# Performance work log

Measured on AMD Instinct MI355X. Metric: run time of the kernel, lower is better.

The kernel has to match this reference:

```python
import jax, jax.numpy as jnp
import numpy as np

K = 3          # kernel size
STRIDE = 1
PAD = 1
DIL = 1


def setup_inputs() -> dict:
    key = jax.random.key(0)
    k1, k2, k3 = jax.random.split(key, 3)
    N, Cin, H, W = 8, 128, 64, 64
    Cout = 128
    x = jax.random.normal(k1, (N, Cin, H, W), dtype=jnp.float32)
    # offset channels: 2 * deformable_groups * K*K = 18, interleaved (dy, dx) per tap
    offset = jax.random.normal(k2, (N, 2 * K * K, H, W), dtype=jnp.float32)
    weight = jax.random.normal(k3, (Cout, Cin, K, K), dtype=jnp.float32) / np.sqrt(Cin * K * K)
    return {"x": x, "offset": offset, "weight": weight}


def _deform_conv(x, offset, weight):
    N, Cin, H, W = x.shape
    Cout = weight.shape[0]
    KK = K * K
    Ho, Wo = offset.shape[2], offset.shape[3]

    off = offset.reshape(N, KK, 2, Ho, Wo)
    dy = off[:, :, 0]  # [N, KK, Ho, Wo]
    dx = off[:, :, 1]

    kh = jnp.repeat(jnp.arange(K), K).astype(x.dtype)   # [KK]
    kw = jnp.tile(jnp.arange(K), K).astype(x.dtype)     # [KK]
    base_i = (jnp.arange(Ho) * STRIDE - PAD).astype(x.dtype)  # [Ho]
    base_j = (jnp.arange(Wo) * STRIDE - PAD).astype(x.dtype)  # [Wo]

    # Sampling positions: [N, KK, Ho, Wo]
    py = base_i[None, None, :, None] + (kh * DIL)[None, :, None, None] + dy
    px = base_j[None, None, None, :] + (kw * DIL)[None, :, None, None] + dx

    y0 = jnp.floor(py)
    x0 = jnp.floor(px)
    wy1 = py - y0
    wx1 = px - x0
    wy0 = 1.0 - wy1
    wx0 = 1.0 - wx1
    y0i = y0.astype(jnp.int32)
    x0i = x0.astype(jnp.int32)
    y1i = y0i + 1
    x1i = x0i + 1

    x_flat = x.reshape(N, Cin, H * W)

    def gather(yi, xi):
        # zero-padding outside the image
        mask = ((yi >= 0) & (yi < H) & (xi >= 0) & (xi < W)).astype(x.dtype)
        idx = jnp.clip(yi, 0, H - 1) * W + jnp.clip(xi, 0, W - 1)  # [N,KK,Ho,Wo]
        v = jnp.take_along_axis(x_flat, idx.reshape(N, 1, -1), axis=2)  # [N,Cin,KK*Ho*Wo]
        v = v.reshape(N, Cin, KK, Ho, Wo)
        return v * mask[:, None]

    sampled = (gather(y0i, x0i) * (wy0 * wx0)[:, None]
               + gather(y0i, x1i) * (wy0 * wx1)[:, None]
               + gather(y1i, x0i) * (wy1 * wx0)[:, None]
               + gather(y1i, x1i) * (wy1 * wx1)[:, None])  # [N,Cin,KK,Ho,Wo]

    w = weight.reshape(Cout, Cin, KK)
    return jnp.einsum('nckij,ock->noij', sampled, w)


def reference(x, offset, weight):
    return _deform_conv(x, offset, weight)
```

## Files before the change

kernel.cpp:

```cpp
#include <hip/hip_runtime.h>


#define H  64
#define W  64
#define CIN 128
#define COUT 128
#define NB 8
#define KK 9

typedef short bf16x8 __attribute__((ext_vector_type(8)));
typedef float f32x4  __attribute__((ext_vector_type(4)));

__device__ __forceinline__ unsigned short f2bf(float f) {
    unsigned u = __builtin_bit_cast(unsigned, f);
    u += 0x7FFFu + ((u >> 16) & 1u);
    return (unsigned short)(u >> 16);
}
__device__ __forceinline__ float lo_f(unsigned u) { return __builtin_bit_cast(float, u << 16); }
__device__ __forceinline__ float hi_f(unsigned u) { return __builtin_bit_cast(float, u & 0xFFFF0000u); }

__global__ void prep_weight(const float* __restrict__ w, unsigned short* __restrict__ wt) {
    int idx = blockIdx.x * 256 + threadIdx.x;
    if (idx >= KK * COUT * CIN) return;
    int kk = idx / (COUT * CIN);
    int r  = idx - kk * (COUT * CIN);
    int co = r >> 7;
    int c  = r & 127;
    wt[idx] = f2bf(w[(co * CIN + c) * KK + kk]);
}

__global__ void prep_x(const float* __restrict__ x, unsigned short* __restrict__ xt) {
    __shared__ float tile[CIN][W + 1];
    int b = blockIdx.x;
    int n = b >> 6, y = b & 63;
    int t = threadIdx.x;
    int l = t & 63, g = t >> 6;
    const float* src = x + ((size_t)n * CIN * H + y) * W;
    #pragma unroll
    for (int i = 0; i < 32; ++i) {
        int c = g * 32 + i;
        tile[c][l] = src[(size_t)c * H * W + l];
    }
    __syncthreads();
    int xp = t >> 2;
    int cb = (t & 3) * 32;
    unsigned short* dst = xt + (((size_t)(n * H + y) * W + xp) * CIN + cb);
    unsigned rr[16];
    #pragma unroll
    for (int i = 0; i < 16; ++i) {
        float v0 = tile[cb + 2 * i][xp];
        float v1 = tile[cb + 2 * i + 1][xp];
        rr[i] = (unsigned)f2bf(v0) | ((unsigned)f2bf(v1) << 16);
    }
    #pragma unroll
    for (int i = 0; i < 4; ++i)
        ((uint4*)dst)[i] = make_uint4(rr[4*i], rr[4*i+1], rr[4*i+2], rr[4*i+3]);
}

__global__ __launch_bounds__(512, 4) void deform_main(
        const float* __restrict__ offs, const unsigned short* __restrict__ xt,
        const unsigned short* __restrict__ wt, float* __restrict__ out) {
    __shared__ __attribute__((aligned(16))) unsigned short samp[64][CIN + 8];
    __shared__ __attribute__((aligned(16))) unsigned short wts[COUT][CIN + 8];

    int b = blockIdx.x;
    int n = b >> 6, ho = b & 63;
    int t = threadIdx.x;
    int lane = t & 63, wv = t >> 6;
    int lm = lane & 15, lq = lane >> 4;
    int prow = ((wv >> 1) << 4) + lm;
    int cobase = (wv & 1) << 6;

    f32x4 acc[4] = {{0,0,0,0},{0,0,0,0},{0,0,0,0},{0,0,0,0}};

    int p  = t >> 3;
    int cb = (t & 7) << 4;
    const float* offbase = offs + (((size_t)n * 2 * KK) * H + ho) * W + p;

    for (int kk = 0; kk < KK; ++kk) {
        {
            int co = t >> 2;
            int ch = (t & 3) << 5;
            const uint4* src = (const uint4*)(wt + (((size_t)kk * COUT + co) << 7) + ch);
            uint4* dst = (uint4*)&wts[co][ch];
            #pragma unroll
            for (int i = 0; i < 4; ++i) dst[i] = src[i];
        }
        {
            float dy = offbase[(size_t)(2 * kk) * H * W];
            float dx = offbase[(size_t)(2 * kk + 1) * H * W];
            float py = (float)(ho - 1 + kk / 3) + dy;
            float px = (float)(p  - 1 + kk % 3) + dx;
            float y0f = floorf(py), x0f = floorf(px);
            float wy1 = py - y0f, wx1 = px - x0f;
            float wy0 = 1.f - wy1, wx0 = 1.f - wx1;
            int y0 = (int)y0f, x0 = (int)x0f;
            int y1 = y0 + 1, x1 = x0 + 1;
            bool vy0 = (unsigned)y0 < (unsigned)H, vy1 = (unsigned)y1 < (unsigned)H;
            bool vx0 = (unsigned)x0 < (unsigned)W, vx1 = (unsigned)x1 < (unsigned)W;
            float w00 = (vy0 && vx0) ? wy0 * wx0 : 0.f;
            float w01 = (vy0 && vx1) ? wy0 * wx1 : 0.f;
            float w10 = (vy1 && vx0) ? wy1 * wx0 : 0.f;
            float w11 = (vy1 && vx1) ? wy1 * wx1 : 0.f;
            int yc0 = min(max(y0, 0), H - 1), yc1 = min(max(y1, 0), H - 1);
            int xc0 = min(max(x0, 0), W - 1), xc1 = min(max(x1, 0), W - 1);
            const unsigned short* r0 = xt + (size_t)(n * H + yc0) * W * CIN + cb;
            const unsigned short* r1 = xt + (size_t)(n * H + yc1) * W * CIN + cb;
            const unsigned short* b00 = r0 + xc0 * CIN;
            const unsigned short* b01 = r0 + xc1 * CIN;
            const unsigned short* b10 = r1 + xc0 * CIN;
            const unsigned short* b11 = r1 + xc1 * CIN;
            #pragma unroll
            for (int j = 0; j < 2; ++j) {
                uint4 q00 = *(const uint4*)(b00 + 8 * j);
                uint4 q01 = *(const uint4*)(b01 + 8 * j);
                uint4 q10 = *(const uint4*)(b10 + 8 * j);
                uint4 q11 = *(const uint4*)(b11 + 8 * j);
                const unsigned* a0 = (const unsigned*)&q00;
                const unsigned* a1 = (const unsigned*)&q01;
                const unsigned* a2 = (const unsigned*)&q10;
                const unsigned* a3 = (const unsigned*)&q11;
                unsigned rr[4];
                #pragma unroll
                for (int i = 0; i < 4; ++i) {
                    float v0 = w00*lo_f(a0[i]) + w01*lo_f(a1[i]) + w10*lo_f(a2[i]) + w11*lo_f(a3[i]);
                    float v1 = w00*hi_f(a0[i]) + w01*hi_f(a1[i]) + w10*hi_f(a2[i]) + w11*hi_f(a3[i]);
                    rr[i] = (unsigned)f2bf(v0) | ((unsigned)f2bf(v1) << 16);
                }
                *(uint4*)&samp[p][cb + 8 * j] = make_uint4(rr[0], rr[1], rr[2], rr[3]);
            }
        }
        __syncthreads();
        #pragma unroll
        for (int ct = 0; ct < 4; ++ct) {
            bf16x8 a = *(const bf16x8*)&samp[prow][(ct << 5) + (lq << 3)];
            #pragma unroll
            for (int nt = 0; nt < 4; ++nt) {
                bf16x8 bf = *(const bf16x8*)&wts[cobase + (nt << 4) + lm][(ct << 5) + (lq << 3)];
                acc[nt] = __builtin_amdgcn_mfma_f32_16x16x32_bf16(a, bf, acc[nt], 0, 0, 0);
            }
        }
        __syncthreads();
    }
    int wo = ((wv >> 1) << 4) + (lq << 2);
    #pragma unroll
    for (int nt = 0; nt < 4; ++nt) {
        int co = cobase + (nt << 4) + lm;
        *(f32x4*)(out + (((size_t)(n * COUT + co) * H + ho) * W + wo)) = acc[nt];
    }
}

extern "C" void kernel_launch(void* const* d_in, const int* in_sizes, int n_in,
                              void* d_out, int out_size, void* d_ws, size_t ws_size,
                              hipStream_t stream) {
    const float* x      = (const float*)d_in[0];
    const float* offset = (const float*)d_in[1];
    const float* weight = (const float*)d_in[2];
    float* out = (float*)d_out;

    unsigned short* xt = (unsigned short*)d_ws;
    unsigned short* wt = (unsigned short*)((char*)d_ws + (size_t)NB*H*W*CIN*2);

    hipLaunchKernelGGL(prep_weight, dim3((KK*COUT*CIN + 255) / 256), dim3(256), 0, stream,
                       weight, wt);
    hipLaunchKernelGGL(prep_x, dim3(NB * H), dim3(256), 0, stream, x, xt);
    hipLaunchKernelGGL(deform_main, dim3(NB * H), dim3(512), 0, stream,
                       offset, xt, wt, out);
}
```

Baseline: 112.5 us.

## Pre-swizzle weights into MFMA fragment layout and double-buffer sampled tile

Weights are pre-packed into the per-lane MFMA B-fragment layout so the main kernel reads them directly from global/L2 instead of staging a weight tile in LDS each tap. The sampled-activation LDS buffer is double-buffered, which removes one barrier per tap, and the next tap's offsets are prefetched. Blocks are halved to 256 threads covering 32 output columns, which doubles the grid and cuts LDS use to raise occupancy. In exchange, each block re-reads the weights from cache, and the prep_x store pattern is changed.

```diff
diff --git a/kernel.cpp b/kernel.cpp
--- a/kernel.cpp
+++ b/kernel.cpp
@@ -19,14 +19,20 @@
 __device__ __forceinline__ float lo_f(unsigned u) { return __builtin_bit_cast(float, u << 16); }
 __device__ __forceinline__ float hi_f(unsigned u) { return __builtin_bit_cast(float, u & 0xFFFF0000u); }
 
-__global__ void prep_weight(const float* __restrict__ w, unsigned short* __restrict__ wt) {
-    int idx = blockIdx.x * 256 + threadIdx.x;
-    if (idx >= KK * COUT * CIN) return;
-    int kk = idx / (COUT * CIN);
-    int r  = idx - kk * (COUT * CIN);
-    int co = r >> 7;
-    int c  = r & 127;
-    wt[idx] = f2bf(w[(co * CIN + c) * KK + kk]);
+__global__ void prep_weight(const float* __restrict__ w, unsigned short* __restrict__ wtf) {
+    int id = blockIdx.x * 256 + threadIdx.x;
+    int lane = id & 63;
+    int ct = (id >> 6) & 3;
+    int nt = (id >> 8) & 7;
+    int kk = id >> 11;
+    if (kk >= KK) return;
+    int co = nt * 16 + (lane & 15);
+    int c0 = ct * 32 + (lane >> 4) * 8;
+    unsigned short v[8];
+    #pragma unroll
+    for (int j = 0; j < 8; ++j)
+        v[j] = f2bf(w[((size_t)co * CIN + c0 + j) * KK + kk]);
+    *(uint4*)(wtf + (size_t)id * 8) = *(const uint4*)v;
 }
 
 __global__ void prep_x(const float* __restrict__ x, unsigned short* __restrict__ xt) {
@@ -42,111 +48,111 @@
         tile[c][l] = src[(size_t)c * H * W + l];
     }
     __syncthreads();
-    int xp = t >> 2;
-    int cb = (t & 3) * 32;
+    int xp = t & 63;
+    int cb = (t >> 6) * 32;
     unsigned short* dst = xt + (((size_t)(n * H + y) * W + xp) * CIN + cb);
     unsigned rr[16];
     #pragma unroll
     for (int i = 0; i < 16; ++i) {
-        float v0 = tile[cb + 2 * i][xp];
-        float v1 = tile[cb + 2 * i + 1][xp];
-        rr[i] = (unsigned)f2bf(v0) | ((unsigned)f2bf(v1) << 16);
+        rr[i] = (unsigned)f2bf(tile[cb + 2 * i][xp])
+              | ((unsigned)f2bf(tile[cb + 2 * i + 1][xp]) << 16);
     }
     #pragma unroll
     for (int i = 0; i < 4; ++i)
         ((uint4*)dst)[i] = make_uint4(rr[4*i], rr[4*i+1], rr[4*i+2], rr[4*i+3]);
 }
 
-__global__ __launch_bounds__(512, 4) void deform_main(
+__global__ __launch_bounds__(256, 4) void deform_main(
         const float* __restrict__ offs, const unsigned short* __restrict__ xt,
-        const unsigned short* __restrict__ wt, float* __restrict__ out) {
-    __shared__ __attribute__((aligned(16))) unsigned short samp[64][CIN + 8];
-    __shared__ __attribute__((aligned(16))) unsigned short wts[COUT][CIN + 8];
+        const unsigned short* __restrict__ wtf, float* __restrict__ out) {
+    __shared__ __attribute__((aligned(16))) unsigned short samp[2][32][CIN + 8];
 
-    int b = blockIdx.x;
-    int n = b >> 6, ho = b & 63;
+    int b  = blockIdx.x;
+    int hh = b & 1;
+    int ho = (b >> 1) & 63;
+    int n  = b >> 7;
     int t = threadIdx.x;
     int lane = t & 63, wv = t >> 6;
     int lm = lane & 15, lq = lane >> 4;
-    int prow = ((wv >> 1) << 4) + lm;
-    int cobase = (wv & 1) << 6;
+
+    int pl = t >> 3;
+    int cb = (t & 7) << 4;
+    int wo_s = (hh << 5) + pl;
+
+    const float* offp = offs + (((size_t)n * 2 * KK) * H + ho) * W + wo_s;
+    const unsigned short* xbase = xt + (size_t)n * H * W * CIN + cb;
 
     f32x4 acc[4] = {{0,0,0,0},{0,0,0,0},{0,0,0,0},{0,0,0,0}};
 
-    int p  = t >> 3;
-    int cb = (t & 7) << 4;
-    const float* offbase = offs + (((size_t)n * 2 * KK) * H + ho) * W + p;
-
+    float dy = offp[0];
+    float dx = offp[(size_t)H * W];
+    int kh = 0, kw = 0;
     for (int kk = 0; kk < KK; ++kk) {
-        {
-            int co = t >> 2;
-            int ch = (t & 3) << 5;
-            const uint4* src = (const uint4*)(wt + (((size_t)kk * COUT + co) << 7) + ch);
-            uint4* dst = (uint4*)&wts[co][ch];
+        float py = (float)(ho - 1 + kh) + dy;
+        float px = (float)(wo_s - 1 + kw) + dx;
+        float y0f = floorf(py), x0f = floorf(px);
+        float wy1 = py - y0f, wx1 = px - x0f;
+        float wy0 = 1.f - wy1, wx0 = 1.f - wx1;
+        int y0 = (int)y0f, x0 = (int)x0f;
+        int y1 = y0 + 1, x1 = x0 + 1;
+        bool vy0 = (unsigned)y0 < (unsigned)H, vy1 = (unsigned)y1 < (unsigned)H;
+        bool vx0 = (unsigned)x0 < (unsigned)W, vx1 = (unsigned)x1 < (unsigned)W;
+        float w00 = (vy0 && vx0) ? wy0 * wx0 : 0.f;
+        float w01 = (vy0 && vx1) ? wy0 * wx1 : 0.f;
+        float w10 = (vy1 && vx0) ? wy1 * wx0 : 0.f;
+        float w11 = (vy1 && vx1) ? wy1 * wx1 : 0.f;
+        int yc0 = min(max(y0, 0), H - 1), yc1 = min(max(y1, 0), H - 1);
+        int xc0 = min(max(x0, 0), W - 1), xc1 = min(max(x1, 0), W - 1);
+        const unsigned short* r0 = xbase + (size_t)yc0 * (W * CIN);
+        const unsigned short* r1 = xbase + (size_t)yc1 * (W * CIN);
+        const unsigned short* b00 = r0 + (xc0 << 7);
+        const unsigned short* b01 = r0 + (xc1 << 7);
+        const unsigned short* b10 = r1 + (xc0 << 7);
+        const unsigned short* b11 = r1 + (xc1 << 7);
+        unsigned short* dst = &samp[kk & 1][pl][cb];
+        #pragma unroll
+        for (int j = 0; j < 2; ++j) {
+            uint4 q00 = *(const uint4*)(b00 + 8 * j);
+            uint4 q01 = *(const uint4*)(b01 + 8 * j);
+            uint4 q10 = *(const uint4*)(b10 + 8 * j);
+            uint4 q11 = *(const uint4*)(b11 + 8 * j);
+            const unsigned* a0 = (const unsigned*)&q00;
+            const unsigned* a1 = (const unsigned*)&q01;
+            const unsigned* a2 = (const unsigned*)&q10;
+            const unsigned* a3 = (const unsigned*)&q11;
+            unsigned rr[4];
             #pragma unroll
-            for (int i = 0; i < 4; ++i) dst[i] = src[i];
+            for (int i = 0; i < 4; ++i) {
+                float v0 = w00*lo_f(a0[i]) + w01*lo_f(a1[i]) + w10*lo_f(a2[i]) + w11*lo_f(a3[i]);
+                float v1 = w00*hi_f(a0[i]) + w01*hi_f(a1[i]) + w10*hi_f(a2[i]) + w11*hi_f(a3[i]);
+                rr[i] = (unsigned)f2bf(v0) | ((unsigned)f2bf(v1) << 16);
+            }
+            *(uint4*)(dst + 8 * j) = make_uint4(rr[0], rr[1], rr[2], rr[3]);
         }
-        {
-            float dy = offbase[(size_t)(2 * kk) * H * W];
-            float dx = offbase[(size_t)(2 * kk + 1) * H * W];
-            float py = (float)(ho - 1 + kk / 3) + dy;
-            float px = (float)(p  - 1 + kk % 3) + dx;
-            float y0f = floorf(py), x0f = floorf(px);
-            float wy1 = py - y0f, wx1 = px - x0f;
-            float wy0 = 1.f - wy1, wx0 = 1.f - wx1;
-            int y0 = (int)y0f, x0 = (int)x0f;
-            int y1 = y0 + 1, x1 = x0 + 1;
-            bool vy0 = (unsigned)y0 < (unsigned)H, vy1 = (unsigned)y1 < (unsigned)H;
-            bool vx0 = (unsigned)x0 < (unsigned)W, vx1 = (unsigned)x1 < (unsigned)W;
-            float w00 = (vy0 && vx0) ? wy0 * wx0 : 0.f;
-            float w01 = (vy0 && vx1) ? wy0 * wx1 : 0.f;
-            float w10 = (vy1 && vx0) ? wy1 * wx0 : 0.f;
-            float w11 = (vy1 && vx1) ? wy1 * wx1 : 0.f;
-            int yc0 = min(max(y0, 0), H - 1), yc1 = min(max(y1, 0), H - 1);
-            int xc0 = min(max(x0, 0), W - 1), xc1 = min(max(x1, 0), W - 1);
-            const unsigned short* r0 = xt + (size_t)(n * H + yc0) * W * CIN + cb;
-            const unsigned short* r1 = xt + (size_t)(n * H + yc1) * W * CIN + cb;
-            const unsigned short* b00 = r0 + xc0 * CIN;
-            const unsigned short* b01 = r0 + xc1 * CIN;
-            const unsigned short* b10 = r1 + xc0 * CIN;
-            const unsigned short* b11 = r1 + xc1 * CIN;
+        if (kk < KK - 1) {
+            dy = offp[(size_t)(2 * kk + 2) * H * W];
+            dx = offp[(size_t)(2 * kk + 3) * H * W];
+        }
+        ++kw; if (kw == 3) { kw = 0; ++kh; }
+        __syncthreads();
+        const unsigned short* arow = &samp[kk & 1][((wv & 1) << 4) + lm][lq << 3];
+        const unsigned short* wk = wtf + (size_t)kk * 16384
+                                       + ((size_t)(wv >> 1) << 4) * 512 + (lane << 3);
+        #pragma unroll
+        for (int ct = 0; ct < 4; ++ct) {
+            bf16x8 a = *(const bf16x8*)(arow + (ct << 5));
             #pragma unroll
-            for (int j = 0; j < 2; ++j) {
-                uint4 q00 = *(const uint4*)(b00 + 8 * j);
-                uint4 q01 = *(const uint4*)(b01 + 8 * j);
-                uint4 q10 = *(const uint4*)(b10 + 8 * j);
-                uint4 q11 = *(const uint4*)(b11 + 8 * j);
-                const unsigned* a0 = (const unsigned*)&q00;
-                const unsigned* a1 = (const unsigned*)&q01;
-                const unsigned* a2 = (const unsigned*)&q10;
-                const unsigned* a3 = (const unsigned*)&q11;
-                unsigned rr[4];
-                #pragma unroll
-                for (int i = 0; i < 4; ++i) {
-                    float v0 = w00*lo_f(a0[i]) + w01*lo_f(a1[i]) + w10*lo_f(a2[i]) + w11*lo_f(a3[i]);
-                    float v1 = w00*hi_f(a0[i]) + w01*hi_f(a1[i]) + w10*hi_f(a2[i]) + w11*hi_f(a3[i]);
-                    rr[i] = (unsigned)f2bf(v0) | ((unsigned)f2bf(v1) << 16);
-                }
-                *(uint4*)&samp[p][cb + 8 * j] = make_uint4(rr[0], rr[1], rr[2], rr[3]);
+            for (int i = 0; i < 4; ++i) {
+                bf16x8 bf = *(const bf16x8*)(wk + ((i << 2) + ct) * 512);
+                acc[i] = __builtin_amdgcn_mfma_f32_16x16x32_bf16(a, bf, acc[i], 0, 0, 0);
             }
         }
-        __syncthreads();
-        #pragma unroll
-        for (int ct = 0; ct < 4; ++ct) {
-            bf16x8 a = *(const bf16x8*)&samp[prow][(ct << 5) + (lq << 3)];
-            #pragma unroll
-            for (int nt = 0; nt < 4; ++nt) {
-                bf16x8 bf = *(const bf16x8*)&wts[cobase + (nt << 4) + lm][(ct << 5) + (lq << 3)];
-                acc[nt] = __builtin_amdgcn_mfma_f32_16x16x32_bf16(a, bf, acc[nt], 0, 0, 0);
-            }
-        }
-        __syncthreads();
     }
-    int wo = ((wv >> 1) << 4) + (lq << 2);
+    int wo = (hh << 5) + ((wv & 1) << 4) + (lq << 2);
     #pragma unroll
-    for (int nt = 0; nt < 4; ++nt) {
-        int co = cobase + (nt << 4) + lm;
-        *(f32x4*)(out + (((size_t)(n * COUT + co) * H + ho) * W + wo)) = acc[nt];
+    for (int i = 0; i < 4; ++i) {
+        int co = ((wv >> 1) << 6) + (i << 4) + lm;
+        *(f32x4*)(out + (((size_t)(n * COUT + co) * H + ho) * W + wo)) = acc[i];
     }
 }
 
@@ -158,12 +164,11 @@
     const float* weight = (const float*)d_in[2];
     float* out = (float*)d_out;
 
-    unsigned short* xt = (unsigned short*)d_ws;
-    unsigned short* wt = (unsigned short*)((char*)d_ws + (size_t)NB*H*W*CIN*2);
+    unsigned short* xt  = (unsigned short*)d_ws;
+    unsigned short* wtf = (unsigned short*)((char*)d_ws + (size_t)NB*H*W*CIN*2);
 
-    hipLaunchKernelGGL(prep_weight, dim3((KK*COUT*CIN + 255) / 256), dim3(256), 0, stream,
-                       weight, wt);
+    hipLaunchKernelGGL(prep_weight, dim3(72), dim3(256), 0, stream, weight, wtf);
     hipLaunchKernelGGL(prep_x, dim3(NB * H), dim3(256), 0, stream, x, xt);
-    hipLaunchKernelGGL(deform_main, dim3(NB * H), dim3(512), 0, stream,
-                       offset, xt, wt, out);
+    hipLaunchKernelGGL(deform_main, dim3(NB * H * 2), dim3(256), 0, stream,
+                       offset, xt, wtf, out);
 }
```

After: 112.9 us. About the same (+0.3%).
